# Optimization experiments

Hardware: AMD Instinct MI355X
Metric: run time of the kernel (lower is better)

## Reference

```python
import jax, jax.numpy as jnp
import numpy as np

B, S, D, H = 16, 1024, 1024, 16
HD = D // H  # head_dim = 64
SCALE = HD ** -0.5


def setup_inputs() -> dict:
    key = jax.random.key(0)
    ks = jax.random.split(key, 9)
    init = 1.0 / np.sqrt(D)
    x = jax.random.normal(ks[0], (B, S, D), dtype=jnp.float32)
    Wq = jax.random.normal(ks[1], (D, D), dtype=jnp.float32) * init
    bq = jnp.zeros((D,), dtype=jnp.float32)
    Wk = jax.random.normal(ks[2], (D, D), dtype=jnp.float32) * init
    bk = jnp.zeros((D,), dtype=jnp.float32)
    Wv = jax.random.normal(ks[3], (D, D), dtype=jnp.float32) * init
    bv = jnp.zeros((D,), dtype=jnp.float32)
    Wo = jax.random.normal(ks[4], (D, D), dtype=jnp.float32) * init
    bo = jnp.zeros((D,), dtype=jnp.float32)
    return {"x": x, "Wq": Wq, "bq": bq, "Wk": Wk, "bk": bk,
            "Wv": Wv, "bv": bv, "Wo": Wo, "bo": bo}


def reference(x, Wq, bq, Wk, bk, Wv, bv, Wo, bo):
    # QKV projections: [B,S,D] -> [B,H,S,HD]
    def split_heads(t):
        return t.reshape(B, S, H, HD).transpose(0, 2, 1, 3)

    q = split_heads(x @ Wq + bq)
    k = split_heads(x @ Wk + bk)
    v = split_heads(x @ Wv + bv)

    # scores [B,H,S,S]; softmax in fp32 then cast back (matches torch dtype=float32)
    scores = jnp.einsum("bhqd,bhkd->bhqk", q, k) * SCALE
    attn = jax.nn.softmax(scores.astype(jnp.float32), axis=-1).astype(q.dtype)
    # dropout p=0.0 -> identity

    out = jnp.einsum("bhqk,bhkd->bhqd", attn, v)  # [B,H,S,HD]
    out = out.transpose(0, 2, 1, 3).reshape(B, S, D)
    out = out @ Wo + bo
    return out, attn
```

## Files before the change

### kernel.cpp

```cpp
#include <hip/hip_runtime.h>
#include <hip/hip_bf16.h>
#include <cstddef>

#define Bsz 16
#define Ssz 1024
#define Dsz 1024
#define Hn  16
#define HDs 64
#define SCALE_F 0.125f

typedef unsigned short ushort_t;
typedef __bf16 bf16x8 __attribute__((ext_vector_type(8)));
typedef float f32x4 __attribute__((ext_vector_type(4)));
typedef ushort_t u16x4 __attribute__((ext_vector_type(4)));

#define MFMA16(a, b, c) __builtin_amdgcn_mfma_f32_16x16x32_bf16((a), (b), (c), 0, 0, 0)

__device__ inline ushort_t bf16u(float f) {
    __bf16 h = (__bf16)f;
    return __builtin_bit_cast(ushort_t, h);
}

__device__ inline void gld_lds16(const void* g, void* l) {
    __builtin_amdgcn_global_load_lds(
        (const __attribute__((address_space(1))) unsigned int*)g,
        (__attribute__((address_space(3))) unsigned int*)l, 16, 0, 0);
}

__global__ __launch_bounds__(256) void cast_k(const float* __restrict__ in,
                                              ushort_t* __restrict__ o, size_t n)
{
    size_t i = ((size_t)blockIdx.x * 256 + threadIdx.x) * 8;
    if (i >= n) return;
    float4 a = *(const float4*)(in + i);
    float4 b = *(const float4*)(in + i + 4);
    union { ushort_t u[8]; uint4 v; } pk;
    pk.u[0] = bf16u(a.x); pk.u[1] = bf16u(a.y); pk.u[2] = bf16u(a.z); pk.u[3] = bf16u(a.w);
    pk.u[4] = bf16u(b.x); pk.u[5] = bf16u(b.y); pk.u[6] = bf16u(b.z); pk.u[7] = bf16u(b.w);
    *(uint4*)(o + i) = pk.v;
}

__global__ __launch_bounds__(256) void wtrans_k(const float* __restrict__ W,
                                                ushort_t* __restrict__ Wt)
{
    __shared__ float t_[32][33];
    const int tx = threadIdx.x, ty = threadIdx.y;
    const int n0 = blockIdx.x * 32, k0 = blockIdx.y * 32;
    #pragma unroll
    for (int i = 0; i < 4; ++i)
        t_[ty + i * 8][tx] = W[(size_t)(k0 + ty + i * 8) * Dsz + n0 + tx];
    __syncthreads();
    #pragma unroll
    for (int i = 0; i < 4; ++i)
        Wt[(size_t)(n0 + ty + i * 8) * Dsz + k0 + tx] = bf16u(t_[tx][ty + i * 8]);
}

template <int MODE>
__global__ __launch_bounds__(256) void gemm_bt_k(
    const ushort_t* __restrict__ A, const ushort_t* __restrict__ Bt,
    const float* __restrict__ b0, const float* __restrict__ b1,
    const float* __restrict__ b2,
    void* __restrict__ o0, void* __restrict__ o1, void* __restrict__ o2,
    int M, int N, int K)
{
    __shared__ ushort_t As[128 * 32];
    __shared__ ushort_t Bs[128 * 32];

    const int tid = threadIdx.x;
    const int lane = tid & 63;
    const int wv = tid >> 6;
    const int wr = wv >> 1, wc = wv & 1;
    const int bm = blockIdx.y * 128, bn = blockIdx.x * 128;

    const int srw = tid >> 2;
    const int gc = (tid & 3) ^ ((srw >> 1) & 3);
    const ushort_t* aptr0 = A + (size_t)(bm + srw) * K + gc * 8;
    const ushort_t* aptr1 = A + (size_t)(bm + 64 + srw) * K + gc * 8;
    const ushort_t* bptr0 = Bt + (size_t)(bn + srw) * K + gc * 8;
    const ushort_t* bptr1 = Bt + (size_t)(bn + 64 + srw) * K + gc * 8;
    ushort_t* lA0 = As + tid * 8;
    ushort_t* lA1 = As + 2048 + tid * 8;
    ushort_t* lB0 = Bs + tid * 8;
    ushort_t* lB1 = Bs + 2048 + tid * 8;

    const int am = lane & 15;
    const int rc = lane >> 4;
    const int aslot = rc ^ ((am >> 1) & 3);
    const int rrow_a = wr * 64 + am;
    const int rrow_b = wc * 64 + am;

    f32x4 acc[4][4] = {};

    for (int k0 = 0; k0 < K; k0 += 32) {
        if (k0) __syncthreads();
        gld_lds16(aptr0, lA0); gld_lds16(aptr1, lA1);
        gld_lds16(bptr0, lB0); gld_lds16(bptr1, lB1);
        aptr0 += 32; aptr1 += 32; bptr0 += 32; bptr1 += 32;
        __syncthreads();

        bf16x8 af[4], bfr[4];
        #pragma unroll
        for (int m = 0; m < 4; ++m)
            af[m] = *reinterpret_cast<const bf16x8*>(&As[(rrow_a + m * 16) * 32 + aslot * 8]);
        #pragma unroll
        for (int n = 0; n < 4; ++n)
            bfr[n] = *reinterpret_cast<const bf16x8*>(&Bs[(rrow_b + n * 16) * 32 + aslot * 8]);
        #pragma unroll
        for (int m = 0; m < 4; ++m)
            #pragma unroll
            for (int n = 0; n < 4; ++n)
                acc[m][n] = MFMA16(af[m], bfr[n], acc[m][n]);
    }

    const int erow = rc * 4;

    if constexpr (MODE == 0) {
        float* C = (float*)o0;
        #pragma unroll
        for (int m = 0; m < 4; ++m) {
            #pragma unroll
            for (int n = 0; n < 4; ++n) {
                const int col = bn + wc * 64 + n * 16 + am;
                const float bv = b0[col];
                #pragma unroll
                for (int r = 0; r < 4; ++r) {
                    const int row = bm + wr * 64 + m * 16 + erow + r;
                    C[(size_t)row * N + col] = acc[m][n][r] + bv;
                }
            }
        }
    } else {
        const int tsel = bn >> 10;
        const float* bias = (tsel == 0) ? b0 : (tsel == 1) ? b1 : b2;
        ushort_t* dst = (ushort_t*)((tsel == 0) ? o0 : (tsel == 1) ? o1 : o2);
        #pragma unroll
        for (int m = 0; m < 4; ++m) {
            const int row0 = bm + wr * 64 + m * 16 + erow;
            const int b_ = row0 >> 10;
            const int srow0 = row0 & 1023;
            #pragma unroll
            for (int n = 0; n < 4; ++n) {
                const int col = bn + wc * 64 + n * 16 + am;
                const int c1 = col & 1023;
                const int h = c1 >> 6, d = c1 & 63;
                const float bv = bias[c1];
                const size_t hb = ((size_t)(b_ * 16 + h)) << 16;
                if (tsel == 0) {
                    #pragma unroll
                    for (int r = 0; r < 4; ++r)
                        dst[hb + (size_t)(srow0 + r) * 64 + d] =
                            bf16u(acc[m][n][r] + bv);
                } else if (tsel == 1) {
                    const size_t base = hb + (size_t)(srow0 >> 4) * 1024
                                      + (d >> 5) * 512
                                      + (((d >> 3) & 3) * 16 + (srow0 & 15)) * 8
                                      + (d & 7);
                    #pragma unroll
                    for (int r = 0; r < 4; ++r)
                        dst[base + r * 8] = bf16u(acc[m][n][r] + bv);
                } else {
                    const size_t base = hb + (size_t)(d >> 4) * 16384
                                      + (srow0 >> 5) * 512
                                      + (((srow0 >> 3) & 3) * 16 + (d & 15)) * 8
                                      + (srow0 & 7);
                    u16x4 pk;
                    pk.x = bf16u(acc[m][n][0] + bv);
                    pk.y = bf16u(acc[m][n][1] + bv);
                    pk.z = bf16u(acc[m][n][2] + bv);
                    pk.w = bf16u(acc[m][n][3] + bv);
                    *(u16x4*)&dst[base] = pk;
                }
            }
        }
    }
}

__global__ __launch_bounds__(256, 4) void attn_fused_k(
    const ushort_t* __restrict__ Qh, const ushort_t* __restrict__ Kp,
    const ushort_t* __restrict__ Vp, float* __restrict__ attn,
    ushort_t* __restrict__ ctx)
{
    __shared__ ushort_t Pl[16 * 1024];
    __shared__ float ssum[4][16];
    __shared__ float invb[16];

    const int tid = threadIdx.x;
    const int lane = tid & 63;
    const int wv = tid >> 6;
    const int am = lane & 15;
    const int ak = lane >> 4;
    const int kb = wv * 256;

    const int wg = blockIdx.x;
    const int swz = (wg & 7) * 2048 + (wg >> 3);
    const int bh = swz >> 6;
    const int q0 = (swz & 63) << 4;
    const int b = bh >> 4, h = bh & 15;
    const size_t hb = (size_t)bh << 16;

    const ushort_t* qptr = Qh + hb + (size_t)(q0 + am) * 64 + ak * 8;
    const bf16x8 qf0 = *(const bf16x8*)qptr;
    const bf16x8 qf1 = *(const bf16x8*)(qptr + 32);

    f32x4 acc[16];
    #pragma unroll
    for (int n = 0; n < 16; ++n) acc[n] = (f32x4){0.f, 0.f, 0.f, 0.f};

    const ushort_t* kt = Kp + hb + (size_t)(wv * 16) * 1024 + lane * 8;
    __builtin_amdgcn_s_setprio(1);
    #pragma unroll
    for (int n = 0; n < 16; ++n) {
        const bf16x8 kf0 = *(const bf16x8*)(kt + n * 1024);
        const bf16x8 kf1 = *(const bf16x8*)(kt + n * 1024 + 512);
        acc[n] = MFMA16(kf0, qf0, acc[n]);
        acc[n] = MFMA16(kf1, qf1, acc[n]);
    }
    __builtin_amdgcn_s_setprio(0);

    float s = 0.f;
    #pragma unroll
    for (int n = 0; n < 16; ++n)
        #pragma unroll
        for (int r = 0; r < 4; ++r) {
            const float e = __expf(fminf(acc[n][r] * SCALE_F, 60.0f));
            acc[n][r] = e;
            s += e;
        }
    s += __shfl_xor(s, 16);
    s += __shfl_xor(s, 32);
    if (ak == 0) ssum[wv][am] = s;

    char* prow = (char*)Pl + am * 2048;
    const int xr = (am & 7) << 4;
    #pragma unroll
    for (int n = 0; n < 16; ++n) {
        u16x4 pk;
        pk.x = bf16u(acc[n][0]); pk.y = bf16u(acc[n][1]);
        pk.z = bf16u(acc[n][2]); pk.w = bf16u(acc[n][3]);
        *(u16x4*)(prow + (((kb + n * 16 + ak * 4) * 2) ^ xr)) = pk;
    }
    __syncthreads();

    const float inv = 1.0f / (ssum[0][am] + ssum[1][am] + ssum[2][am] + ssum[3][am]);
    if (wv == 0 && ak == 0) invb[am] = inv;

    float* aout = attn + ((size_t)bh * Ssz + q0 + am) * Ssz + kb + ak * 4;
    #pragma unroll
    for (int n = 0; n < 16; ++n) {
        f32x4 v;
        v[0] = acc[n][0] * inv; v[1] = acc[n][1] * inv;
        v[2] = acc[n][2] * inv; v[3] = acc[n][3] * inv;
        __builtin_nontemporal_store(v, (f32x4*)(aout + n * 16));
    }

    f32x4 po = {0.f, 0.f, 0.f, 0.f};
    const ushort_t* vt = Vp + hb + (size_t)wv * 16384 + lane * 8;
    bf16x8 v0 = *(const bf16x8*)(vt);
    bf16x8 v1 = *(const bf16x8*)(vt + 512);
    bf16x8 v2 = *(const bf16x8*)(vt + 1024);
    bf16x8 v3 = *(const bf16x8*)(vt + 1536);
    __builtin_amdgcn_s_setprio(1);
    #pragma unroll
    for (int w = 0; w < 32; w += 4) {
        const bf16x8 p0 = *(const bf16x8*)(prow + (((w + 0) * 64 + ak * 16) ^ xr));
        const bf16x8 p1 = *(const bf16x8*)(prow + (((w + 1) * 64 + ak * 16) ^ xr));
        const bf16x8 p2 = *(const bf16x8*)(prow + (((w + 2) * 64 + ak * 16) ^ xr));
        const bf16x8 p3 = *(const bf16x8*)(prow + (((w + 3) * 64 + ak * 16) ^ xr));
        po = MFMA16(p0, v0, po);
        if (w + 4 < 32) v0 = *(const bf16x8*)(vt + (w + 4) * 512);
        po = MFMA16(p1, v1, po);
        if (w + 5 < 32) v1 = *(const bf16x8*)(vt + (w + 5) * 512);
        po = MFMA16(p2, v2, po);
        if (w + 6 < 32) v2 = *(const bf16x8*)(vt + (w + 6) * 512);
        po = MFMA16(p3, v3, po);
        if (w + 7 < 32) v3 = *(const bf16x8*)(vt + (w + 7) * 512);
    }
    __builtin_amdgcn_s_setprio(0);
    __syncthreads();

    #pragma unroll
    for (int r = 0; r < 4; ++r) {
        const float v = po[r] * invb[ak * 4 + r];
        ctx[((size_t)b * Ssz + q0 + ak * 4 + r) * Dsz + h * HDs + wv * 16 + am] = bf16u(v);
    }
}

extern "C" void kernel_launch(void* const* d_in, const int* in_sizes, int n_in,
                              void* d_out, int out_size, void* d_ws, size_t ws_size,
                              hipStream_t stream)
{
    const float* x  = (const float*)d_in[0];
    const float* Wq = (const float*)d_in[1];
    const float* bq = (const float*)d_in[2];
    const float* Wk = (const float*)d_in[3];
    const float* bk = (const float*)d_in[4];
    const float* Wv = (const float*)d_in[5];
    const float* bv = (const float*)d_in[6];
    const float* Wo = (const float*)d_in[7];
    const float* bo = (const float*)d_in[8];

    const size_t BSD = (size_t)Bsz * Ssz * Dsz;
    const size_t WSZ = (size_t)Dsz * Dsz;

    float* outp = (float*)d_out;
    float* attn = outp + BSD;

    ushort_t* xbf  = (ushort_t*)d_ws;
    ushort_t* Qh   = xbf + BSD;
    ushort_t* Kp   = Qh + BSD;
    ushort_t* Vp   = Kp + BSD;
    ushort_t* ctxb = Vp + BSD;
    ushort_t* Wqkv = ctxb + BSD;
    ushort_t* Wot  = Wqkv + 3 * WSZ;

    const int M = Bsz * Ssz;

    cast_k<<<dim3((unsigned)(BSD / 2048)), 256, 0, stream>>>(x, xbf, BSD);

    dim3 tblk(32, 8);
    dim3 tgrd(32, 32);
    wtrans_k<<<tgrd, tblk, 0, stream>>>(Wq, Wqkv);
    wtrans_k<<<tgrd, tblk, 0, stream>>>(Wk, Wqkv + WSZ);
    wtrans_k<<<tgrd, tblk, 0, stream>>>(Wv, Wqkv + 2 * WSZ);
    wtrans_k<<<tgrd, tblk, 0, stream>>>(Wo, Wot);

    gemm_bt_k<1><<<dim3(24, 128), 256, 0, stream>>>(
        xbf, Wqkv, bq, bk, bv, Qh, Kp, Vp, M, 3072, Dsz);

    attn_fused_k<<<dim3(16384), 256, 0, stream>>>(Qh, Kp, Vp, attn, ctxb);

    gemm_bt_k<0><<<dim3(8, 128), 256, 0, stream>>>(
        ctxb, Wot, bo, nullptr, nullptr, outp, nullptr, nullptr, M, Dsz, Dsz);
}
```

Measured before the change: 550.0 us.

## Stage Q/K epilogue through LDS for coalesced stores, fold scale into Q, merge transposes

The QKV GEMM epilogue for the Q and K tiles now writes results transposed into shared memory, then emits 16-byte coalesced global stores instead of scattered 2-byte stores. The softmax scale is applied to Q in the projection epilogue rather than per score in the attention kernel. The four weight transpose launches are merged into one launch using blockIdx.z. The staging adds barriers and a larger shared-memory buffer in the MODE 1 GEMM, which may reduce occupancy. Q is now rounded to bf16 after scaling, which slightly changes rounding.

```diff
diff --git a/kernel.cpp b/kernel.cpp
--- a/kernel.cpp
+++ b/kernel.cpp
@@ -13,6 +13,7 @@
 typedef __bf16 bf16x8 __attribute__((ext_vector_type(8)));
 typedef float f32x4 __attribute__((ext_vector_type(4)));
 typedef ushort_t u16x4 __attribute__((ext_vector_type(4)));
+typedef ushort_t u16x8 __attribute__((ext_vector_type(8)));
 
 #define MFMA16(a, b, c) __builtin_amdgcn_mfma_f32_16x16x32_bf16((a), (b), (c), 0, 0, 0)
 
@@ -40,12 +41,17 @@
     *(uint4*)(o + i) = pk.v;
 }
 
-__global__ __launch_bounds__(256) void wtrans_k(const float* __restrict__ W,
-                                                ushort_t* __restrict__ Wt)
+__global__ __launch_bounds__(256) void wtrans_k(
+    const float* __restrict__ W0, const float* __restrict__ W1,
+    const float* __restrict__ W2, const float* __restrict__ W3,
+    ushort_t* __restrict__ T012, ushort_t* __restrict__ T3)
 {
     __shared__ float t_[32][33];
     const int tx = threadIdx.x, ty = threadIdx.y;
     const int n0 = blockIdx.x * 32, k0 = blockIdx.y * 32;
+    const int z = blockIdx.z;
+    const float* W = (z == 0) ? W0 : (z == 1) ? W1 : (z == 2) ? W2 : W3;
+    ushort_t* Wt = (z < 3) ? (T012 + (size_t)z * Dsz * Dsz) : T3;
     #pragma unroll
     for (int i = 0; i < 4; ++i)
         t_[ty + i * 8][tx] = W[(size_t)(k0 + ty + i * 8) * Dsz + n0 + tx];
@@ -63,8 +69,9 @@
     void* __restrict__ o0, void* __restrict__ o1, void* __restrict__ o2,
     int M, int N, int K)
 {
-    __shared__ ushort_t As[128 * 32];
-    __shared__ ushort_t Bs[128 * 32];
+    __shared__ ushort_t shmem[MODE == 1 ? 128 * 132 : 128 * 64];
+    ushort_t* As = shmem;
+    ushort_t* Bs = shmem + 128 * 32;
 
     const int tid = threadIdx.x;
     const int lane = tid & 63;
@@ -133,32 +140,20 @@
         const int tsel = bn >> 10;
         const float* bias = (tsel == 0) ? b0 : (tsel == 1) ? b1 : b2;
         ushort_t* dst = (ushort_t*)((tsel == 0) ? o0 : (tsel == 1) ? o1 : o2);
-        #pragma unroll
-        for (int m = 0; m < 4; ++m) {
-            const int row0 = bm + wr * 64 + m * 16 + erow;
-            const int b_ = row0 >> 10;
-            const int srow0 = row0 & 1023;
-            #pragma unroll
-            for (int n = 0; n < 4; ++n) {
-                const int col = bn + wc * 64 + n * 16 + am;
-                const int c1 = col & 1023;
-                const int h = c1 >> 6, d = c1 & 63;
-                const float bv = bias[c1];
-                const size_t hb = ((size_t)(b_ * 16 + h)) << 16;
-                if (tsel == 0) {
-                    #pragma unroll
-                    for (int r = 0; r < 4; ++r)
-                        dst[hb + (size_t)(srow0 + r) * 64 + d] =
-                            bf16u(acc[m][n][r] + bv);
-                } else if (tsel == 1) {
-                    const size_t base = hb + (size_t)(srow0 >> 4) * 1024
-                                      + (d >> 5) * 512
-                                      + (((d >> 3) & 3) * 16 + (srow0 & 15)) * 8
-                                      + (d & 7);
-                    #pragma unroll
-                    for (int r = 0; r < 4; ++r)
-                        dst[base + r * 8] = bf16u(acc[m][n][r] + bv);
-                } else {
+        const int bnm = bn & 1023;
+
+        if (tsel == 2) {
+            #pragma unroll
+            for (int m = 0; m < 4; ++m) {
+                const int row0 = bm + wr * 64 + m * 16 + erow;
+                const int b_ = row0 >> 10;
+                const int srow0 = row0 & 1023;
+                #pragma unroll
+                for (int n = 0; n < 4; ++n) {
+                    const int c1 = bnm + wc * 64 + n * 16 + am;
+                    const int h = c1 >> 6, d = c1 & 63;
+                    const float bv = bias[c1];
+                    const size_t hb = ((size_t)(b_ * 16 + h)) << 16;
                     const size_t base = hb + (size_t)(d >> 4) * 16384
                                       + (srow0 >> 5) * 512
                                       + (((srow0 >> 3) & 3) * 16 + (d & 15)) * 8
@@ -171,6 +166,56 @@
                     *(u16x4*)&dst[base] = pk;
                 }
             }
+        } else {
+            __syncthreads();
+            #pragma unroll
+            for (int m = 0; m < 4; ++m) {
+                const int srow = wr * 64 + m * 16 + erow;
+                #pragma unroll
+                for (int n = 0; n < 4; ++n) {
+                    const int ccol = wc * 64 + n * 16 + am;
+                    const float bv = bias[bnm + ccol];
+                    u16x4 pk;
+                    if (tsel == 0) {
+                        pk.x = bf16u((acc[m][n][0] + bv) * SCALE_F);
+                        pk.y = bf16u((acc[m][n][1] + bv) * SCALE_F);
+                        pk.z = bf16u((acc[m][n][2] + bv) * SCALE_F);
+                        pk.w = bf16u((acc[m][n][3] + bv) * SCALE_F);
+                    } else {
+                        pk.x = bf16u(acc[m][n][0] + bv);
+                        pk.y = bf16u(acc[m][n][1] + bv);
+                        pk.z = bf16u(acc[m][n][2] + bv);
+                        pk.w = bf16u(acc[m][n][3] + bv);
+                    }
+                    *(u16x4*)&shmem[ccol * 132 + srow] = pk;
+                }
+            }
+            __syncthreads();
+            #pragma unroll
+            for (int j = 0; j < 8; ++j) {
+                const int idx = j * 256 + tid;
+                const int s  = idx >> 4;
+                const int c8 = idx & 15;
+                union { ushort_t u[8]; uint4 v; } pk;
+                #pragma unroll
+                for (int e = 0; e < 8; ++e)
+                    pk.u[e] = shmem[(c8 * 8 + e) * 132 + s];
+                const int row = bm + s;
+                const int b_ = row >> 10;
+                const int srow0 = row & 1023;
+                const int h = (bnm >> 6) + (c8 >> 3);
+                const int d0 = (c8 & 7) * 8;
+                const size_t hb = ((size_t)(b_ * 16 + h)) << 16;
+                size_t gaddr;
+                if (tsel == 0) {
+                    gaddr = hb + (size_t)srow0 * 64 + d0;
+                } else {
+                    gaddr = hb + (size_t)(srow0 >> 4) * 1024
+                          + (d0 >> 5) * 512
+                          + (((d0 >> 3) & 3) * 16 + (srow0 & 15)) * 8;
+                }
+                *(uint4*)&dst[gaddr] = pk.v;
+            }
         }
     }
 }
@@ -222,7 +267,7 @@
     for (int n = 0; n < 16; ++n)
         #pragma unroll
         for (int r = 0; r < 4; ++r) {
-            const float e = __expf(fminf(acc[n][r] * SCALE_F, 60.0f));
+            const float e = __expf(fminf(acc[n][r], 60.0f));
             acc[n][r] = e;
             s += e;
         }
@@ -317,12 +362,8 @@
 
     cast_k<<<dim3((unsigned)(BSD / 2048)), 256, 0, stream>>>(x, xbf, BSD);
 
-    dim3 tblk(32, 8);
-    dim3 tgrd(32, 32);
-    wtrans_k<<<tgrd, tblk, 0, stream>>>(Wq, Wqkv);
-    wtrans_k<<<tgrd, tblk, 0, stream>>>(Wk, Wqkv + WSZ);
-    wtrans_k<<<tgrd, tblk, 0, stream>>>(Wv, Wqkv + 2 * WSZ);
-    wtrans_k<<<tgrd, tblk, 0, stream>>>(Wo, Wot);
+    wtrans_k<<<dim3(32, 32, 4), dim3(32, 8), 0, stream>>>(
+        Wq, Wk, Wv, Wo, Wqkv, Wot);
 
     gemm_bt_k<1><<<dim3(24, 128), 256, 0, stream>>>(
         xbf, Wqkv, bq, bk, bv, Qh, Kp, Vp, M, 3072, Dsz);
```

After: 542.4 us. No clear change (-1.4%).
